# Kernel optimization log

Measured on AMD Instinct MI355X. Metric: run time of the kernel, lower is better.

Reference implementation:

```python
import jax, jax.numpy as jnp
import numpy as np

EPS = 1e-8  # torch F.cosine_similarity norm clamp
TEMPERATURE = 0.05


def setup_inputs() -> dict:
    key = jax.random.key(0)
    k1, k2 = jax.random.split(key)
    N, D = 8192, 768
    query_embeddings = jax.random.normal(k1, (N, D), dtype=jnp.float32)
    content_embeddings = jax.random.normal(k2, (N, D), dtype=jnp.float32)
    return {"query_embeddings": query_embeddings, "content_embeddings": content_embeddings}


def reference(query_embeddings, content_embeddings):
    # cosine_similarity(q[:,None], c[None,:], dim=2) == normalize(q) @ normalize(c).T
    qn = query_embeddings / jnp.maximum(
        jnp.linalg.norm(query_embeddings, axis=-1, keepdims=True), EPS)
    cn = content_embeddings / jnp.maximum(
        jnp.linalg.norm(content_embeddings, axis=-1, keepdims=True), EPS)
    sim = jnp.einsum('nd,md->nm', qn, cn) / TEMPERATURE  # [N, N]
    # cross-entropy with targets = arange(N): positive is the diagonal
    logz = jax.nn.logsumexp(sim, axis=-1)                # [N]
    loss = jnp.mean(logz - jnp.diagonal(sim))
    return loss
```

## Files before the change

### kernel.cpp

```cpp
#include <hip/hip_runtime.h>
#include <hip/hip_bf16.h>


#define NROWS 8192
#define DDIM  768
#define ROWB  1536
#define NKT  (DDIM / 64)
#define NIT  (NKT / 2)
#define GRID_T (NROWS / 256)

constexpr float INV_TEMP = 20.0f;
constexpr float NORM_EPS = 1e-8f;

using bf16 = __hip_bfloat16;
typedef __attribute__((ext_vector_type(4))) float  f32x4;
typedef __attribute__((ext_vector_type(8))) short  bf16x8;

__global__ void norm_diag_kernel(const float* __restrict__ q, const float* __restrict__ c,
                                 bf16* __restrict__ qn, bf16* __restrict__ cn,
                                 float* __restrict__ diag) {
    const int row  = (blockIdx.x * 256 + threadIdx.x) >> 6;
    const int lane = threadIdx.x & 63;
    const float4* qv = (const float4*)(q + (size_t)row * DDIM);
    const float4* cv = (const float4*)(c + (size_t)row * DDIM);
    float4 a[3], b[3];
    #pragma unroll
    for (int j = 0; j < 3; ++j) { a[j] = qv[lane + j * 64]; b[j] = cv[lane + j * 64]; }
    float ssq = 0.f, ssc = 0.f, dot = 0.f;
    #pragma unroll
    for (int j = 0; j < 3; ++j) {
        ssq += a[j].x * a[j].x + a[j].y * a[j].y + a[j].z * a[j].z + a[j].w * a[j].w;
        ssc += b[j].x * b[j].x + b[j].y * b[j].y + b[j].z * b[j].z + b[j].w * b[j].w;
        dot += a[j].x * b[j].x + a[j].y * b[j].y + a[j].z * b[j].z + a[j].w * b[j].w;
    }
    #pragma unroll
    for (int m = 32; m; m >>= 1) {
        ssq += __shfl_xor(ssq, m);
        ssc += __shfl_xor(ssc, m);
        dot += __shfl_xor(dot, m);
    }
    float invq = 1.0f / fmaxf(sqrtf(ssq), NORM_EPS);
    float invc = 1.0f / fmaxf(sqrtf(ssc), NORM_EPS);
    if (lane == 0) diag[row] = dot * invq * invc * INV_TEMP;
    ushort4* qo = (ushort4*)(qn + (size_t)row * DDIM);
    ushort4* co = (ushort4*)(cn + (size_t)row * DDIM);
    #pragma unroll
    for (int j = 0; j < 3; ++j) {
        union { ushort4 u; bf16 h[4]; } oq, oc;
        oq.h[0] = __float2bfloat16(a[j].x * invq); oq.h[1] = __float2bfloat16(a[j].y * invq);
        oq.h[2] = __float2bfloat16(a[j].z * invq); oq.h[3] = __float2bfloat16(a[j].w * invq);
        oc.h[0] = __float2bfloat16(b[j].x * invc); oc.h[1] = __float2bfloat16(b[j].y * invc);
        oc.h[2] = __float2bfloat16(b[j].z * invc); oc.h[3] = __float2bfloat16(b[j].w * invc);
        qo[lane + j * 64] = oq.u;
        co[lane + j * 64] = oc.u;
    }
}

__device__ __forceinline__ void async16(void* l, const void* g) {
    __builtin_amdgcn_global_load_lds(
        (const __attribute__((address_space(1))) void*)g,
        (__attribute__((address_space(3))) void*)l, 16, 0, 0);
}

#define BARRIER __builtin_amdgcn_s_barrier()
#define SCHED0  __builtin_amdgcn_sched_barrier(0)
#define PRIO1   __builtin_amdgcn_s_setprio(1)
#define PRIO0   __builtin_amdgcn_s_setprio(0)
#define VMCNT(n) do { asm volatile("s_waitcnt vmcnt(" #n ")" ::: "memory"); SCHED0; } while (0)

#define STAGE_A(P, H, KT) do {                                              \
    const char* _g = aG + (size_t)(H) * 128 * ROWB + (size_t)(KT) * 128;    \
    char* _l = lds + (P) * 65536 + (H) * 16384 + dstW;                      \
    async16(_l, _g);                                                        \
    async16(_l + 8192, _g + 64 * ROWB);                                     \
} while (0)
#define STAGE_B(P, H, KT) do {                                              \
    const char* _g = bG + (size_t)(H) * 128 * ROWB + (size_t)(KT) * 128;    \
    char* _l = lds + 32768 + (P) * 65536 + (H) * 16384 + dstW;              \
    async16(_l, _g);                                                        \
    async16(_l + 8192, _g + 64 * ROWB);                                     \
} while (0)

#define READ_A(P, MH) do {                                                  \
    const char* _ab = lds + (P) * 65536 + aBaseT + (MH) * 64 * 128;         \
    _Pragma("unroll") for (int mi = 0; mi < 4; ++mi) {                      \
        a[mi][0] = *(const bf16x8*)(_ab + mi * 2048 + xk0);                 \
        a[mi][1] = *(const bf16x8*)(_ab + mi * 2048 + xk1);                 \
    }                                                                       \
} while (0)
#define READ_B(P, NH) do {                                                  \
    const char* _bb = lds + 32768 + (P) * 65536 + bBaseT + (NH) * 32 * 128; \
    _Pragma("unroll") for (int ni = 0; ni < 2; ++ni) {                      \
        bfr[NH][ni][0] = *(const bf16x8*)(_bb + ni * 2048 + xk0);           \
        bfr[NH][ni][1] = *(const bf16x8*)(_bb + ni * 2048 + xk1);           \
    }                                                                       \
} while (0)

#define MFMA_Q(MH, NH)                                                      \
    _Pragma("unroll") for (int mi = 0; mi < 4; ++mi)                        \
    _Pragma("unroll") for (int ni = 0; ni < 2; ++ni) {                      \
        acc[(MH)*4+mi][(NH)*2+ni] = __builtin_amdgcn_mfma_f32_16x16x32_bf16(\
            a[mi][0], bfr[NH][ni][0], acc[(MH)*4+mi][(NH)*2+ni], 0, 0, 0);  \
        acc[(MH)*4+mi][(NH)*2+ni] = __builtin_amdgcn_mfma_f32_16x16x32_bf16(\
            a[mi][1], bfr[NH][ni][1], acc[(MH)*4+mi][(NH)*2+ni], 0, 0, 0);  \
    }

__launch_bounds__(512, 2)
__global__ void simgemm_kernel(const bf16* __restrict__ A, const bf16* __restrict__ B,
                               float* __restrict__ partial) {
    __shared__ __attribute__((aligned(16))) char smem[131072];
    char* lds = smem;

    const int bid = blockIdx.x;
    const int swz = (bid & 7) * 128 + (bid >> 3);
    const int st = swz >> 5, within = swz & 31;
    const int tm = (st >> 3) * 8 + (within & 7);
    const int tn = (st & 7) * 4 + (within >> 3);
    const int rowBase = tm * 256, colBase = tn * 256;
    const int tid = threadIdx.x;
    const int wid = tid >> 6, lane = tid & 63;
    const int wr = wid >> 2, wc = wid & 3;

    const int sr  = tid >> 3;
    const int scb = ((tid & 7) * 16) ^ ((sr & 7) << 4);
    const char* aG = (const char*)A + (size_t)(rowBase + sr) * ROWB + scb;
    const char* bG = (const char*)B + (size_t)(colBase + sr) * ROWB + scb;
    const int dstW = wid * 1024;

    const int aBaseT = wr * 16384 + (lane & 15) * 128;
    const int bBaseT = (wc >> 1) * 16384 + ((wc & 1) * 64 + (lane & 15)) * 128;
    const int klane  = (lane >> 4) * 16;
    const int swzr   = (lane & 7) << 4;
    const int xk0    = klane ^ swzr;
    const int xk1    = (64 + klane) ^ swzr;

    f32x4  acc[8][4] = {};
    bf16x8 a[4][2];
    bf16x8 bfr[2][2][2];

    STAGE_A(0, 0, 0); STAGE_A(0, 1, 0);
    STAGE_B(0, 0, 0); STAGE_B(0, 1, 0);
    STAGE_A(1, 0, 1); STAGE_A(1, 1, 1);
    VMCNT(4);
    BARRIER; SCHED0;

    for (int i = 0; i < NIT; ++i) {
        const int t1 = 2 * i + 1;
        const int t2 = 2 * i + 2, t3 = 2 * i + 3;
        const bool more = (i + 1 < NIT);
        READ_A(0, 0); READ_B(0, 0);
        STAGE_B(1, 0, t1);
        BARRIER; PRIO1; MFMA_Q(0, 0); PRIO0; BARRIER; SCHED0;
        READ_B(0, 1);
        STAGE_B(1, 1, t1);
        BARRIER; PRIO1; MFMA_Q(0, 1); PRIO0; BARRIER; SCHED0;
        READ_A(0, 1);
        if (more) STAGE_A(0, 0, t2);
        BARRIER; PRIO1; MFMA_Q(1, 0); PRIO0; BARRIER; SCHED0;
        if (more) STAGE_A(0, 1, t2);
        BARRIER; PRIO1; MFMA_Q(1, 1); PRIO0;
        if (more) { VMCNT(4); } else { VMCNT(0); }
        BARRIER; SCHED0;
        READ_A(1, 0); READ_B(1, 0);
        if (more) STAGE_B(0, 0, t2);
        BARRIER; PRIO1; MFMA_Q(0, 0); PRIO0; BARRIER; SCHED0;
        READ_B(1, 1);
        if (more) STAGE_B(0, 1, t2);
        BARRIER; PRIO1; MFMA_Q(0, 1); PRIO0; BARRIER; SCHED0;
        READ_A(1, 1);
        if (more) STAGE_A(1, 0, t3);
        BARRIER; PRIO1; MFMA_Q(1, 0); PRIO0; BARRIER; SCHED0;
        if (more) STAGE_A(1, 1, t3);
        BARRIER; PRIO1; MFMA_Q(1, 1); PRIO0;
        if (more) { VMCNT(4); }
        BARRIER; SCHED0;
    }

    __syncthreads();
    float* red = (float*)smem;
    #pragma unroll
    for (int m = 0; m < 8; ++m) {
        #pragma unroll
        for (int r = 0; r < 4; ++r) {
            float s = 0.f;
            #pragma unroll
            for (int n = 0; n < 4; ++n)
                s += __expf(fmaf(INV_TEMP, acc[m][n][r], -INV_TEMP));
            s += __shfl_xor(s, 1);
            s += __shfl_xor(s, 2);
            s += __shfl_xor(s, 4);
            s += __shfl_xor(s, 8);
            if ((lane & 15) == 0)
                red[(wr * 128 + m * 16 + (lane >> 4) * 4 + r) * 4 + wc] = s;
        }
    }
    __syncthreads();
    if (tid < 256)
        partial[(size_t)(rowBase + tid) * GRID_T + tn] =
            red[tid * 4 + 0] + red[tid * 4 + 1] + red[tid * 4 + 2] + red[tid * 4 + 3];
}

__global__ void finalize_kernel(const float* __restrict__ partial,
                                const float* __restrict__ diag,
                                float* __restrict__ out) {
    int row = blockIdx.x * 256 + threadIdx.x;
    const float4* p = (const float4*)(partial + (size_t)row * GRID_T);
    float z = 0.f;
    #pragma unroll
    for (int i = 0; i < GRID_T / 4; ++i) {
        float4 v = p[i];
        z += v.x + v.y + v.z + v.w;
    }
    float term = INV_TEMP + logf(z) - diag[row];
    #pragma unroll
    for (int m = 32; m; m >>= 1) term += __shfl_xor(term, m);
    __shared__ float wsum[4];
    if ((threadIdx.x & 63) == 0) wsum[threadIdx.x >> 6] = term;
    __syncthreads();
    if (threadIdx.x == 0) {
        float s = wsum[0] + wsum[1] + wsum[2] + wsum[3];
        atomicAdd(out, s * (1.0f / NROWS));
    }
}

extern "C" void kernel_launch(void* const* d_in, const int* in_sizes, int n_in,
                              void* d_out, int out_size, void* d_ws, size_t ws_size,
                              hipStream_t stream) {
    const float* q = (const float*)d_in[0];
    const float* c = (const float*)d_in[1];
    float* out = (float*)d_out;

    char* ws = (char*)d_ws;
    bf16* qn = (bf16*)ws;
    bf16* cn = (bf16*)(ws + (size_t)NROWS * DDIM * 2);
    float* diag = (float*)(ws + (size_t)NROWS * DDIM * 4);
    float* partial = diag + NROWS;

    hipMemsetAsync(d_out, 0, sizeof(float), stream);

    norm_diag_kernel<<<NROWS / 4, 256, 0, stream>>>(q, c, qn, cn, diag);
    simgemm_kernel<<<GRID_T * GRID_T, 512, 0, stream>>>(qn, cn, partial);
    finalize_kernel<<<NROWS / 256, 256, 0, stream>>>(partial, diag, out);
}
```

Before: 193.1 us.

## Restructure GEMM main loop barriers and prefetch first fragments across iterations

Removes the double barriers around each MFMA quarter, leaving a single barrier per phase, and hoists the first LDS fragment reads before the loop so each iteration prefetches the next one's fragments. The vmcnt wait thresholds change from 4 to 6 and are placed differently. The tile swizzle for L2 locality is replaced with a plain row-major block mapping. Fewer barriers should cut synchronisation stalls, but fewer waits risk LDS races if the hazards are not fully covered, and the simpler mapping may lose L2 reuse.

```diff
diff --git a/kernel.cpp b/kernel.cpp
--- a/kernel.cpp
+++ b/kernel.cpp
@@ -66,7 +66,7 @@
 #define SCHED0  __builtin_amdgcn_sched_barrier(0)
 #define PRIO1   __builtin_amdgcn_s_setprio(1)
 #define PRIO0   __builtin_amdgcn_s_setprio(0)
-#define VMCNT(n) do { asm volatile("s_waitcnt vmcnt(" #n ")" ::: "memory"); SCHED0; } while (0)
+#define VMCNT(n) do { asm volatile("s_waitcnt vmcnt(" #n ")" ::: "memory"); } while (0)
 
 #define STAGE_A(P, H, KT) do {                                              \
     const char* _g = aG + (size_t)(H) * 128 * ROWB + (size_t)(KT) * 128;    \
@@ -112,10 +112,7 @@
     char* lds = smem;
 
     const int bid = blockIdx.x;
-    const int swz = (bid & 7) * 128 + (bid >> 3);
-    const int st = swz >> 5, within = swz & 31;
-    const int tm = (st >> 3) * 8 + (within & 7);
-    const int tn = (st & 7) * 4 + (within >> 3);
+    const int tm = bid >> 5, tn = bid & 31;
     const int rowBase = tm * 256, colBase = tn * 256;
     const int tid = threadIdx.x;
     const int wid = tid >> 6, lane = tid & 63;
@@ -143,37 +140,48 @@
     STAGE_A(1, 0, 1); STAGE_A(1, 1, 1);
     VMCNT(4);
     BARRIER; SCHED0;
-
+    READ_A(0, 0); READ_B(0, 0);
+    SCHED0;
+
+    #pragma unroll 1
     for (int i = 0; i < NIT; ++i) {
         const int t1 = 2 * i + 1;
         const int t2 = 2 * i + 2, t3 = 2 * i + 3;
         const bool more = (i + 1 < NIT);
-        READ_A(0, 0); READ_B(0, 0);
         STAGE_B(1, 0, t1);
-        BARRIER; PRIO1; MFMA_Q(0, 0); PRIO0; BARRIER; SCHED0;
-        READ_B(0, 1);
+        PRIO1; MFMA_Q(0, 0); PRIO0;
+        VMCNT(6);
+        BARRIER; SCHED0;
+        READ_B(0, 1); SCHED0;
         STAGE_B(1, 1, t1);
-        BARRIER; PRIO1; MFMA_Q(0, 1); PRIO0; BARRIER; SCHED0;
-        READ_A(0, 1);
+        PRIO1; MFMA_Q(0, 1); PRIO0;
+        BARRIER; SCHED0;
+        READ_A(0, 1); SCHED0;
         if (more) STAGE_A(0, 0, t2);
-        BARRIER; PRIO1; MFMA_Q(1, 0); PRIO0; BARRIER; SCHED0;
+        PRIO1; MFMA_Q(1, 0); PRIO0;
+        BARRIER; SCHED0;
         if (more) STAGE_A(0, 1, t2);
-        BARRIER; PRIO1; MFMA_Q(1, 1); PRIO0;
-        if (more) { VMCNT(4); } else { VMCNT(0); }
-        BARRIER; SCHED0;
-        READ_A(1, 0); READ_B(1, 0);
+        PRIO1; MFMA_Q(1, 1); PRIO0;
+        if (more) { VMCNT(6); } else { VMCNT(0); }
+        BARRIER; SCHED0;
+        READ_A(1, 0); READ_B(1, 0); SCHED0;
         if (more) STAGE_B(0, 0, t2);
-        BARRIER; PRIO1; MFMA_Q(0, 0); PRIO0; BARRIER; SCHED0;
-        READ_B(1, 1);
+        PRIO1; MFMA_Q(0, 0); PRIO0;
+        if (more) { VMCNT(6); }
+        BARRIER; SCHED0;
+        READ_B(1, 1); SCHED0;
         if (more) STAGE_B(0, 1, t2);
-        BARRIER; PRIO1; MFMA_Q(0, 1); PRIO0; BARRIER; SCHED0;
-        READ_A(1, 1);
+        PRIO1; MFMA_Q(0, 1); PRIO0;
+        BARRIER; SCHED0;
+        READ_A(1, 1); SCHED0;
         if (more) STAGE_A(1, 0, t3);
-        BARRIER; PRIO1; MFMA_Q(1, 0); PRIO0; BARRIER; SCHED0;
+        PRIO1; MFMA_Q(1, 0); PRIO0;
+        BARRIER; SCHED0;
         if (more) STAGE_A(1, 1, t3);
-        BARRIER; PRIO1; MFMA_Q(1, 1); PRIO0;
-        if (more) { VMCNT(4); }
-        BARRIER; SCHED0;
+        PRIO1; MFMA_Q(1, 1); PRIO0;
+        if (more) { VMCNT(6); }
+        BARRIER; SCHED0;
+        if (more) { READ_A(0, 0); READ_B(0, 0); SCHED0; }
     }
 
     __syncthreads();
```

Result: no change. 191.2 us (-1.0%).
